# Performance work log

Hardware: AMD Instinct MI355X
Metric: run time of the kernel (lower is better)

Reference implementation:

```python
import jax, jax.numpy as jnp
import numpy as np

DIM = 512
HEADS = 8
DIM_HEAD = 64          # dim // 8
M = 256                # num_landmarks = dim // 2
PINV_ITERS = 6
SCALE = DIM_HEAD ** -0.5
KERNEL = 33            # residual_conv_kernel


def setup_inputs() -> dict:
    key = jax.random.key(0)
    ks = jax.random.split(key, 5)
    b, n = 4, 4096  # n divisible by M -> no padding branch
    inner = HEADS * DIM_HEAD
    x = jax.random.normal(ks[0], (b, n, DIM), jnp.float32)
    ln_w = jnp.ones((DIM,), jnp.float32)
    ln_b = jnp.zeros((DIM,), jnp.float32)
    w_qkv = jax.random.normal(ks[1], (DIM, 3 * inner), jnp.float32) / np.sqrt(DIM)
    w_out = jax.random.normal(ks[2], (inner, DIM), jnp.float32) / np.sqrt(inner)
    b_out = jnp.zeros((DIM,), jnp.float32)
    # depthwise Conv2d(heads, heads, (33,1), groups=heads, bias=False): weight [H,1,33,1]
    w_res = jax.random.normal(ks[3], (HEADS, 1, KERNEL, 1), jnp.float32) * 0.05
    return dict(x=x, ln_w=ln_w, ln_b=ln_b, w_qkv=w_qkv, w_out=w_out, b_out=b_out, w_res=w_res)


def moore_penrose_iter_pinv(x, iters=PINV_ITERS):
    # x: (..., m, m) row-stochastic softmax matrix
    abs_x = jnp.abs(x)
    col = abs_x.sum(-1).max()   # global max, matches torch.max(col)
    row = abs_x.sum(-2).max()
    z = jnp.swapaxes(x, -1, -2) / (col * row)
    I = jnp.eye(x.shape[-1], dtype=x.dtype)
    for _ in range(iters):
        xz = x @ z
        z = 0.25 * z @ (13 * I - xz @ (15 * I - xz @ (7 * I - xz)))
    return z


def reference(x, ln_w, ln_b, w_qkv, w_out, b_out, w_res):
    b, n, d = x.shape
    # pre-norm LayerNorm (eps=1e-5, biased variance)
    mu = x.mean(-1, keepdims=True)
    var = ((x - mu) ** 2).mean(-1, keepdims=True)
    h = (x - mu) * jax.lax.rsqrt(var + 1e-5) * ln_w + ln_b

    qkv = h @ w_qkv                           # (b, n, 3*inner)
    q, k, v = jnp.split(qkv, 3, axis=-1)
    to_heads = lambda t: t.reshape(b, n, HEADS, DIM_HEAD).transpose(0, 2, 1, 3)
    q = to_heads(q) * SCALE                   # (b, h, n, d)
    k = to_heads(k)
    v = to_heads(v)

    # landmarks: mean over consecutive chunks of size l = n // M
    l = n // M
    q_l = q.reshape(b, HEADS, M, l, DIM_HEAD).mean(3)  # (b, h, m, d)
    k_l = k.reshape(b, HEADS, M, l, DIM_HEAD).mean(3)

    sim1 = jnp.einsum('bhid,bhjd->bhij', q, k_l)       # (b, h, n, m)
    sim2 = jnp.einsum('bhid,bhjd->bhij', q_l, k_l)     # (b, h, m, m)
    sim3 = jnp.einsum('bhid,bhjd->bhij', q_l, k)       # (b, h, m, n)
    attn1 = jax.nn.softmax(sim1, -1)
    attn2 = jax.nn.softmax(sim2, -1)
    attn3 = jax.nn.softmax(sim3, -1)

    attn2_inv = moore_penrose_iter_pinv(attn2)
    out = (attn1 @ attn2_inv) @ (attn3 @ v)            # (b, h, n, d)

    # residual depthwise conv over sequence dim, per head
    pad = KERNEL // 2
    res = jax.lax.conv_general_dilated(
        v, w_res, window_strides=(1, 1), padding=((pad, pad), (0, 0)),
        dimension_numbers=('NCHW', 'OIHW', 'NCHW'), feature_group_count=HEADS)
    out = out + res

    out = out.transpose(0, 2, 1, 3).reshape(b, n, HEADS * DIM_HEAD)
    out = out @ w_out + b_out                          # to_out (dropout=identity in eval)
    return x + out
```

## Files before the change

kernel.cpp:

```cpp
#include <hip/hip_runtime.h>
#include <hip/hip_bf16.h>
#include <hip/hip_fp16.h>

#define B_ 4
#define H_ 8
#define N_ 4096
#define DH_ 64
#define D_ 512
#define M_ 256
#define BH_ 32
#define NT_ 16384

typedef unsigned short u16;
using sh8 = __attribute__((ext_vector_type(8))) short;
using sh4 = __attribute__((ext_vector_type(4))) short;
using f4  = __attribute__((ext_vector_type(4))) float;

__device__ __forceinline__ float bf2f(u16 u){ return __uint_as_float(((unsigned)u)<<16); }
__device__ __forceinline__ u16 f2bf(float f){
  unsigned u = __float_as_uint(f);
  u += 0x7fffu + ((u>>16)&1u);
  return (u16)(u>>16);
}

// ... 78 lines not shown
  for (int pass=0; pass<2; pass++){
    __syncthreads();
    if (wr==pass){
      #pragma unroll
      for (int fr=0;fr<4;fr++){
        #pragma unroll
        for (int fc=0;fc<4;fc++){
          #pragma unroll
          for (int j=0;j<4;j++)
            tb[(fr*16+((lane>>4)<<2)+j)*132 + wc*64+fc*16+(lane&15)] = acc[fr][fc][j];
        }
      }
    }
    __syncthreads();
    #pragma unroll
    for (int i=0;i<4;i++){
      int ch = i*256+tid;
      int lr = ch>>4, cq = (ch&15)*8;
      int r = r0 + pass*64 + lr;
      int c = c0 + cq;
      int which = c>>9, hh = (c>>6)&7, d = c&63;
      int bb = r>>12, n = r&4095;
      float scale = (which==0)? 0.125f : 1.f;
      sh8 ov;
      #pragma unroll
      for (int jj=0;jj<8;jj++) ov[jj] = (short)f2bf(tb[lr*132+cq+jj]*scale);
      u16* dst = which==0 ? q : (which==1 ? k : v);
      *(sh8*)(dst + (((size_t)(bb*8+hh))*4096 + n)*64 + d) = ov;
    }
  }
}

__global__ __launch_bounds__(64) void landmark_kernel(const u16* __restrict__ q,
    const u16* __restrict__ k, u16* __restrict__ ql, u16* __restrict__ kl){
  int bh = blockIdx.x, m = blockIdx.y, d = threadIdx.x;
  const u16* qp = q + (((size_t)bh*4096) + m*16)*64 + d;
  const u16* kp = k + (((size_t)bh*4096) + m*16)*64 + d;
  float sq=0, sk=0;
  #pragma unroll
  for (int j=0;j<16;j++){ sq += bf2f(qp[j*64]); sk += bf2f(kp[j*64]); }
  ql[((size_t)bh*256+m)*64+d] = f2bf(sq*(1.f/16.f));
  kl[((size_t)bh*256+m)*64+d] = f2bf(sk*(1.f/16.f));
}

__global__ __launch_bounds__(256) void attn2_kernel(const u16* __restrict__ ql,
    const u16* __restrict__ kl, u16* __restrict__ Xhi, u16* __restrict__ Xlo){
  int bh = blockIdx.x, rb = blockIdx.y;
  __shared__ short klds[256*72];
  const u16* kg = kl + (size_t)bh*256*64;
  int tid = threadIdx.x;
  #pragma unroll
  for (int i=0;i<8;i++){
    int c = i*256+tid, row = c>>3, kgi = c&7;
    *(sh8*)&klds[row*72+kgi*8] = *(const sh8*)(kg + row*64 + kgi*8);
  }
  __syncthreads();
  int r = rb*16 + (tid>>4), t = tid&15;
  const u16* qr = ql + ((size_t)bh*256 + r)*64;
  float qv[64];
  #pragma unroll
  for (int i=0;i<8;i++){
    sh8 v8 = *(const sh8*)(qr + i*8);
    #pragma unroll
    for (int j=0;j<8;j++) qv[i*8+j] = bf2f((u16)v8[j]);
  }
  float s[16];
  #pragma unroll
  for (int j=0;j<16;j++){
    int col = t + 16*j;
    const short* kr = &klds[col*72];
    float accv=0;
    #pragma unroll
    for (int i8=0;i8<8;i8++){
      sh8 kv = *(const sh8*)(kr + i8*8);
      #pragma unroll
      for (int jj=0;jj<8;jj++) accv += qv[i8*8+jj]*bf2f((u16)kv[jj]);
    }
    s[j]=accv;
  }
  float mx = s[0];
  #pragma unroll
  for (int j=1;j<16;j++) mx = fmaxf(mx, s[j]);
  #pragma unroll
  for (int o=1;o<16;o<<=1) mx = fmaxf(mx, __shfl_xor(mx,o));
  float sum=0;
  #pragma unroll
  for (int j=0;j<16;j++){ s[j] = __expf(s[j]-mx); sum += s[j]; }
  #pragma unroll
  for (int o=1;o<16;o<<=1) sum += __shfl_xor(sum,o);
  float inv = 1.f/sum;
  u16* Xh = Xhi + ((size_t)bh*256 + r)*256;
  u16* Xl = Xlo + ((size_t)bh*256 + r)*256;
  #pragma unroll
  for (int j=0;j<16;j++){
    float val = s[j]*inv;
    u16 hb = f2bf(val);
    Xh[t+16*j] = hb; Xl[t+16*j] = f2bf(val - bf2f(hb));
  }
}

__global__ __launch_bounds__(256) void colrow_kernel(const u16* __restrict__ Xhi,
    const u16* __restrict__ Xlo, float* __restrict__ scal){
  int bh = blockIdx.x, t = threadIdx.x;
  const u16* xh = Xhi + (size_t)bh*65536;
  const u16* xl = Xlo + (size_t)bh*65536;
  float cs=0, rs=0;
  for (int m=0;m<256;m++) cs += bf2f(xh[m*256+t]) + bf2f(xl[m*256+t]);
  for (int c=0;c<256;c++) rs += bf2f(xh[t*256+c]) + bf2f(xl[t*256+c]);
  #pragma unroll
  for (int o=32;o;o>>=1){ cs = fmaxf(cs, __shfl_xor(cs,o)); rs = fmaxf(rs, __shfl_xor(rs,o)); }
  __shared__ float sb[4], sb2[4];
  if ((t&63)==0){ sb[t>>6]=cs; sb2[t>>6]=rs; }
  __syncthreads();
  if (t==0){
    float mc = fmaxf(fmaxf(sb[0],sb[1]),fmaxf(sb[2],sb[3]));
    float mr = fmaxf(fmaxf(sb2[0],sb2[1]),fmaxf(sb2[2],sb2[3]));
    atomicMax((unsigned*)&scal[1], __float_as_uint(mc));
    atomicMax((unsigned*)&scal[0], __float_as_uint(mr));
  }
}

__global__ __launch_bounds__(256) void ztinit_kernel(const u16* __restrict__ Xhi,
    const u16* __restrict__ Xlo, const float* __restrict__ scal,
    u16* __restrict__ Zhi, u16* __restrict__ Zlo, u16* __restrict__ ZThi, u16* __restrict__ ZTlo){
  int bh = blockIdx.x; int xr0 = blockIdx.y*64, xc0 = blockIdx.z*64;
  __shared__ float tb[64*66];
  float inv = 1.f/(scal[0]*scal[1]);
  int tid = threadIdx.x;
  size_t mo = (size_t)bh*65536;
  int row = tid>>2, cof = (tid&3)*16;
  #pragma unroll
  for (int s2=0;s2<2;s2++){
    sh8 hv = *(const sh8*)(Xhi + mo + (size_t)(xr0+row)*256 + xc0+cof+s2*8);
    sh8 lv = *(const sh8*)(Xlo + mo + (size_t)(xr0+row)*256 + xc0+cof+s2*8);
    #pragma unroll
    for (int j=0;j<8;j++) tb[row*66 + cof+s2*8+j] = (bf2f((u16)hv[j])+bf2f((u16)lv[j]))*inv;
  }
  __syncthreads();
  int lc = tid&63;
  #pragma unroll
  for (int i=0;i<16;i++){
    int lr = i*4 + (tid>>6);
    float v1 = tb[lr*66+lc];
    u16 h1 = f2bf(v1);
    ZThi[mo + (size_t)(xr0+lr)*256 + xc0+lc] = h1;
    ZTlo[mo + (size_t)(xr0+lr)*256 + xc0+lc] = f2bf(v1 - bf2f(h1));
    float v2 = tb[lc*66+lr];
    u16 h2 = f2bf(v2);
    Zhi[mo + (size_t)(xc0+lr)*256 + xr0+lc] = h2;
    Zlo[mo + (size_t)(xc0+lr)*256 + xr0+lc] = f2bf(v2 - bf2f(h2));
  }
}

__device__ __forceinline__ void pinv_body(
    const u16* __restrict__ Ahi, const u16* __restrict__ Alo,
    const u16* __restrict__ Bthi, const u16* __restrict__ Btlo,
    const u16* __restrict__ E1hi, const u16* __restrict__ E1lo,
    const u16* __restrict__ E2hi, const u16* __restrict__ E2lo,
    u16* __restrict__ Chi, u16* __restrict__ Clo,
    u16* __restrict__ CThi, u16* __restrict__ CTlo,
    float k0, float k1, float k2, int bh, int r0, int col0,
    short* smem){
  size_t mo = (size_t)bh*65536;
  int tid=threadIdx.x, lane=tid&63, w=tid>>6, wr=w>>1, wc=w&1;
  int srow = tid>>2, skof = (tid&3)*8;
  const u16* pA  = Ahi  + mo + (size_t)(r0+srow)*256 + skof;
  const u16* pAl = Alo  + mo + (size_t)(r0+srow)*256 + skof;
  const u16* pB  = Bthi + mo + (size_t)(col0+srow)*256 + skof;
  const u16* pBl = Btlo + mo + (size_t)(col0+srow)*256 + skof;
  float e1v[2][2][4], e2v[2][2][4];
  if (E1hi){
    #pragma unroll
    for (int fr=0;fr<2;fr++){
      #pragma unroll
      for (int fc=0;fc<2;fc++){
        #pragma unroll
        for (int j=0;j<4;j++){
          int lr = wr*32+fr*16+((lane>>4)<<2)+j, lc = wc*32+fc*16+(lane&15);
          size_t o = mo+(size_t)(r0+lr)*256+col0+lc;
          e1v[fr][fc][j] = bf2f(E1hi[o]) + bf2f(E1lo[o]);
        }
      }
    }
  }
  if (E2hi){
    #pragma unroll
    for (int fr=0;fr<2;fr++){
      #pragma unroll
      for (int fc=0;fc<2;fc++){
        #pragma unroll
        for (int j=0;j<4;j++){
          int lr = wr*32+fr*16+((lane>>4)<<2)+j, lc = wc*32+fc*16+(lane&15);
          size_t o = mo+(size_t)(r0+lr)*256+col0+lc;
          e2v[fr][fc][j] = bf2f(E2hi[o]) + bf2f(E2lo[o]);
        }
      }
    }
  }
  sh8 ra  = *(const sh8*)(pA);
  sh8 ral = *(const sh8*)(pAl);
  sh8 rb  = *(const sh8*)(pB);
  sh8 rbl = *(const sh8*)(pBl);
  f4 acc[2][2];
  #pragma unroll
  for (int i=0;i<2;i++){
    #pragma unroll
    for (int j=0;j<2;j++) acc[i][j]=0;
  }
  for (int kt=0;kt<8;kt++){
    short* Ah = smem + (kt&1)*10240;
    short* Al = Ah + 2560; short* Bh = Ah + 5120; short* Bl = Ah + 7680;
    *(sh8*)&Ah[srow*40+skof] = ra;
    *(sh8*)&Al[srow*40+skof] = ral;
    *(sh8*)&Bh[srow*40+skof] = rb;
    *(sh8*)&Bl[srow*40+skof] = rbl;
    __syncthreads();
    if (kt<7){
      int o2 = (kt+1)*32;
      ra  = *(const sh8*)(pA+o2);  ral = *(const sh8*)(pAl+o2);
      rb  = *(const sh8*)(pB+o2);  rbl = *(const sh8*)(pBl+o2);
    }
    sh8 ah[2], al[2], bh8[2], bl8[2];
    #pragma unroll
    for (int fr=0;fr<2;fr++){
      int off = (wr*32+fr*16+(lane&15))*40 + ((lane>>4)<<3);
      ah[fr] = *(const sh8*)&Ah[off]; al[fr] = *(const sh8*)&Al[off];
    }
    #pragma unroll
    for (int fc=0;fc<2;fc++){
      int off = (wc*32+fc*16+(lane&15))*40 + ((lane>>4)<<3);
      bh8[fc] = *(const sh8*)&Bh[off]; bl8[fc] = *(const sh8*)&Bl[off];
    }
    #pragma unroll
    for (int fr=0;fr<2;fr++){
      #pragma unroll
      for (int fc=0;fc<2;fc++){
        acc[fr][fc] = __builtin_amdgcn_mfma_f32_16x16x32_bf16(ah[fr], bh8[fc], acc[fr][fc], 0,0,0);
        acc[fr][fc] = __builtin_amdgcn_mfma_f32_16x16x32_bf16(ah[fr], bl8[fc], acc[fr][fc], 0,0,0);
        acc[fr][fc] = __builtin_amdgcn_mfma_f32_16x16x32_bf16(al[fr], bh8[fc], acc[fr][fc], 0,0,0);
      }
    }
  }
  __syncthreads();
  float* tb = (float*)smem;
  #pragma unroll
  for (int fr=0;fr<2;fr++){
    #pragma unroll
    for (int fc=0;fc<2;fc++){
      #pragma unroll
      for (int j=0;j<4;j++){
        int lr = wr*32+fr*16+((lane>>4)<<2)+j, lc = wc*32+fc*16+(lane&15);
        float val = k0*acc[fr][fc][j];
        if (E1hi) val += k1*e1v[fr][fc][j];
        if (E2hi) val += k2*e2v[fr][fc][j];
        tb[lr*66+lc] = val;
      }
    }
  }
  __syncthreads();
  int lc2 = tid&63;
  #pragma unroll
  for (int i=0;i<16;i++){
    int lr2 = i*4+(tid>>6);
    if (Chi){
      float v1 = tb[lr2*66+lc2];
      u16 hb=f2bf(v1);
      Chi[mo+(size_t)(r0+lr2)*256+col0+lc2]=hb;
      Clo[mo+(size_t)(r0+lr2)*256+col0+lc2]=f2bf(v1-bf2f(hb));
    }
    if (CThi){
      float v2 = tb[lc2*66 + lr2];
      u16 hb2=f2bf(v2);
      CThi[mo+(size_t)(col0+lr2)*256 + r0+lc2]=hb2;
      CTlo[mo+(size_t)(col0+lr2)*256 + r0+lc2]=f2bf(v2-bf2f(hb2));
    }
  }
}

__global__ __launch_bounds__(256) void pinv_mm(
    const u16* Ahi, const u16* Alo, const u16* Bthi, const u16* Btlo,
    const u16* E1hi, const u16* E1lo, const u16* E2hi, const u16* E2lo,
    u16* Chi, u16* Clo, u16* CThi, u16* CTlo,
    float k0, float k1, float k2){
  __shared__ __align__(16) short smem[2*10240];
  pinv_body(Ahi,Alo,Bthi,Btlo,E1hi,E1lo,E2hi,E2lo,Chi,Clo,CThi,CTlo,
            k0,k1,k2, blockIdx.z, blockIdx.x*64, blockIdx.y*64, smem);
}

__global__ __launch_bounds__(256) void pinv_zupd(
    const u16* Zhi, const u16* Zlo, u16* ZnHi, u16* ZnLo,
    const u16* T1hi, const u16* T1lo,
    u16* TnChi, u16* TnClo, u16* TnThi, u16* TnTlo,
    const u16* Bthi, const u16* Btlo){
  __shared__ __align__(16) short smem[2*10240];
  int which = blockIdx.z >> 5, bh = blockIdx.z & 31;
  const u16* Ah = which ? T1hi : Zhi;
  const u16* Al = which ? T1lo : Zlo;
  u16* Ch  = which ? TnChi : ZnHi;
  u16* Cl  = which ? TnClo : ZnLo;
  u16* CTh = which ? TnThi : (u16*)0;
  u16* CTl = which ? TnTlo : (u16*)0;
  pinv_body(Ah,Al,Bthi,Btlo, Ah,Al, (u16*)0,(u16*)0, Ch,Cl,CTh,CTl,
            -0.25f, 3.25f, 0.f, bh, blockIdx.x*64, blockIdx.y*64, smem);
}

__global__ __launch_bounds__(256) void gemm_logits(const u16* __restrict__ Aall,
    const u16* __restrict__ Btall, __half* __restrict__ Oall,
    int N, size_t sA, size_t sB, size_t sO){
  int bh = blockIdx.z;
  const u16* A  = Aall  + (size_t)bh*sA + (size_t)blockIdx.x*128*64;
  const u16* Bt = Btall + (size_t)bh*sB + (size_t)blockIdx.y*128*64;
  __half* O = Oall + (size_t)bh*sO + (size_t)blockIdx.x*128*N + (size_t)blockIdx.y*128;
  __shared__ short As[128*72], Bs[128*72];
  int tid=threadIdx.x, lane=tid&63, w=tid>>6, wr=w>>1, wc=w&1;
  #pragma unroll
  for (int i=0;i<4;i++){
    int c=i*256+tid, row=c>>3, kg=c&7;
    *(sh8*)&As[row*72+kg*8] = *(const sh8*)(A  + (size_t)row*64 + kg*8);
    *(sh8*)&Bs[row*72+kg*8] = *(const sh8*)(Bt + (size_t)row*64 + kg*8);
  }
  __syncthreads();
  f4 acc[4][4];
  #pragma unroll
  for (int i=0;i<4;i++){
    #pragma unroll
    for (int j=0;j<4;j++) acc[i][j]=0;
  }
  #pragma unroll
  for (int kc=0;kc<2;kc++){
    sh8 a[4], bq[4];
    #pragma unroll
    for (int fr=0;fr<4;fr++) a[fr]  = *(const sh8*)&As[(wr*64+fr*16+(lane&15))*72 + kc*32 + ((lane>>4)<<3)];
    #pragma unroll
    for (int fc=0;fc<4;fc++) bq[fc] = *(const sh8*)&Bs[(wc*64+fc*16+(lane&15))*72 + kc*32 + ((lane>>4)<<3)];
    #pragma unroll
    for (int fr=0;fr<4;fr++){
      #pragma unroll
      for (int fc=0;fc<4;fc++)
        acc[fr][fc] = __builtin_amdgcn_mfma_f32_16x16x32_bf16(a[fr], bq[fc], acc[fr][fc], 0,0,0);
    }
  }
  #pragma unroll
  for (int fr=0;fr<4;fr++){
    #pragma unroll
    for (int fc=0;fc<4;fc++){
      #pragma unroll
      for (int j=0;j<4;j++)
        O[(size_t)(wr*64+fr*16+((lane>>4)<<2)+j)*N + wc*64+fc*16+(lane&15)] = __float2half(acc[fr][fc][j]);
    }
  }
}

__global__ __launch_bounds__(256) void stats_kernel(const __half* __restrict__ logits,
    float2* __restrict__ stats, int RL){
  size_t row = blockIdx.x;
  const __half2* p = (const __half2*)(logits + row*RL);
  int t = threadIdx.x, n2 = RL>>1;
  float mx = -1e30f;
  for (int i=t;i<n2;i+=256){ float2 f = __half22float2(p[i]); mx = fmaxf(mx, fmaxf(f.x,f.y)); }
  #pragma unroll
  for (int o=32;o;o>>=1) mx = fmaxf(mx, __shfl_xor(mx,o));
  __shared__ float sb[4], sb2[4];
  if ((t&63)==0) sb[t>>6]=mx;
  __syncthreads();
  mx = fmaxf(fmaxf(sb[0],sb[1]),fmaxf(sb[2],sb[3]));
  float s=0;
  for (int i=t;i<n2;i+=256){ float2 f = __half22float2(p[i]); s += __expf(f.x-mx)+__expf(f.y-mx); }
  #pragma unroll
  for (int o=32;o;o>>=1) s += __shfl_xor(s,o);
  if ((t&63)==0) sb2[t>>6]=s;
  __syncthreads();
  s = sb2[0]+sb2[1]+sb2[2]+sb2[3];
  if (t==0) stats[row] = make_float2(mx, 1.f/s);
}

__global__ __launch_bounds__(256) void gemm_out3(const __half* __restrict__ Lall,
    const float2* __restrict__ stall, const u16* __restrict__ vall, float* __restrict__ part){
  int bh = blockIdx.z, mt = blockIdx.x, ks = blockIdx.y;
  const __half* L = Lall + (size_t)bh*256*4096 + (size_t)mt*128*4096 + (size_t)ks*512;
  const float2* st = stall + (size_t)bh*256 + mt*128;
  const u16* V = vall + (size_t)bh*4096*64 + (size_t)ks*512*64;
  float* O = part + ((size_t)(bh*8+ks)*256 + (size_t)mt*128)*64;
  __shared__ short As[128*72], Bs[64*72];
  int tid=threadIdx.x, lane=tid&63, w=tid>>6;
  f4 acc[2][4];
  #pragma unroll
  for (int i=0;i<2;i++){
    #pragma unroll
    for (int j=0;j<4;j++) acc[i][j]=0;
  }
  for (int kt=0;kt<8;kt++){
    __syncthreads();
    #pragma unroll
    for (int i=0;i<4;i++){
      int c=i*256+tid, row=c>>3, kg=c&7;
      const __half2* src = (const __half2*)(L + (size_t)row*4096 + kt*64 + kg*8);
      float2 ms = st[row];
      sh8 ov;
      #pragma unroll
      for (int jj=0;jj<4;jj++){
        float2 f = __half22float2(src[jj]);
        ov[2*jj]   = (short)f2bf(__expf(f.x-ms.x)*ms.y);
        ov[2*jj+1] = (short)f2bf(__expf(f.y-ms.x)*ms.y);
      }
      *(sh8*)&As[row*72+kg*8] = ov;
    }
    #pragma unroll
    for (int i=0;i<16;i++){
      int c=i*256+tid, d=c&63, nl=c>>6;
      Bs[d*72+nl] = (short)V[(size_t)(kt*64+nl)*64 + d];
    }
    __syncthreads();
    #pragma unroll
    for (int kc=0;kc<2;kc++){
      sh8 a[2], bq[4];
      #pragma unroll
      for (int fr=0;fr<2;fr++) a[fr]  = *(const sh8*)&As[(w*32+fr*16+(lane&15))*72 + kc*32+((lane>>4)<<3)];
      #pragma unroll
      for (int fc=0;fc<4;fc++) bq[fc] = *(const sh8*)&Bs[(fc*16+(lane&15))*72 + kc*32+((lane>>4)<<3)];
      #pragma unroll
      for (int fr=0;fr<2;fr++){
        #pragma unroll
        for (int fc=0;fc<4;fc++)
          acc[fr][fc] = __builtin_amdgcn_mfma_f32_16x16x32_bf16(a[fr], bq[fc], acc[fr][fc], 0,0,0);
      }
    }
  }
  #pragma unroll
  for (int fr=0;fr<2;fr++){
    #pragma unroll
    for (int fc=0;fc<4;fc++){
      #pragma unroll
      for (int j=0;j<4;j++)
        O[(size_t)(w*32+fr*16+((lane>>4)<<2)+j)*64 + fc*16+(lane&15)] = acc[fr][fc][j];
    }
  }
}

__global__ __launch_bounds__(256) void reduce_o3(const float* __restrict__ part, float* __restrict__ o3){
  int idx = blockIdx.x*256+threadIdx.x;
  int bh = idx>>14, rem = idx & 16383;
  float s=0;
  #pragma unroll
  for (int ks=0;ks<8;ks++) s += part[(((size_t)(bh*8+ks))<<14) + rem];
  o3[idx]=s;
}

__global__ __launch_bounds__(256) void wt_kernel(const u16* __restrict__ Zhi,
    const u16* __restrict__ Zlo, const float* __restrict__ o3, u16* __restrict__ Wt){
  int bh = blockIdx.x; int m = blockIdx.y*4 + (threadIdx.x>>6); int d = threadIdx.x&63;
  const u16* zh = Zhi + ((size_t)bh*256 + m)*256;
  const u16* zl = Zlo + ((size_t)bh*256 + m)*256;
  const float* op = o3 + (size_t)bh*256*64 + d;
  float accv = 0;
  for (int kk=0;kk<256;kk++) accv += (bf2f(zh[kk])+bf2f(zl[kk]))*op[kk*64];
  Wt[((size_t)bh*64 + d)*256 + m] = f2bf(accv);
}

__global__ __launch_bounds__(256) void fused_out1(const u16* __restrict__ q,
    const u16* __restrict__ klall, const u16* __restrict__ Wtall, u16* __restrict__ Oall){
  int rb = blockIdx.x, bh = blockIdx.y;
  __shared__ __align__(16) short sm[18432];
  short* Bs = sm; short* P = sm;
  int tid=threadIdx.x, lane=tid&63, w=tid>>6;
  const u16* qb  = q + ((size_t)bh*4096 + (size_t)rb*64)*64;
  const u16* klb = klall + (size_t)bh*256*64;
  const u16* Wt  = Wtall + (size_t)bh*64*256;
  #pragma unroll
  for (int i=0;i<8;i++){
    int c = i*256+tid, row = c>>3, kg = c&7;
    *(sh8*)&Bs[row*72+kg*8] = *(const sh8*)(klb + row*64 + kg*8);
  }
  const u16* qrow = qb + (size_t)(w*16+(lane&15))*64 + ((lane>>4)<<3);
  sh8 a0 = *(const sh8*)(qrow);
  sh8 a1 = *(const sh8*)(qrow + 32);
  __syncthreads();
  f4 acc[16];
  #pragma unroll
  for (int fc=0;fc<16;fc++){
    sh8 b0 = *(const sh8*)&Bs[(fc*16+(lane&15))*72 + ((lane>>4)<<3)];
    sh8 b1 = *(const sh8*)&Bs[(fc*16+(lane&15))*72 + 32 + ((lane>>4)<<3)];
    acc[fc]=0;
    acc[fc] = __builtin_amdgcn_mfma_f32_16x16x32_bf16(a0, b0, acc[fc], 0,0,0);
    acc[fc] = __builtin_amdgcn_mfma_f32_16x16x32_bf16(a1, b1, acc[fc], 0,0,0);
  }
  float inv_[4];
  #pragma unroll
  for (int j=0;j<4;j++){
    float mx=-1e30f;
    #pragma unroll
    for (int fc=0;fc<16;fc++) mx = fmaxf(mx, acc[fc][j]);
    #pragma unroll
    for (int o=1;o<16;o<<=1) mx = fmaxf(mx, __shfl_xor(mx,o));
    float s=0;
    #pragma unroll
    for (int fc=0;fc<16;fc++){ float e=__expf(acc[fc][j]-mx); acc[fc][j]=e; s+=e; }
    #pragma unroll
    for (int o=1;o<16;o<<=1) s += __shfl_xor(s,o);
    inv_[j] = 1.f/s;
  }
  __syncthreads();
  #pragma unroll
  for (int fc=0;fc<16;fc++){
    #pragma unroll
    for (int j=0;j<4;j++){
      int row = w*16 + ((lane>>4)<<2) + j, col = fc*16 + (lane&15);
      P[row*268 + col] = (short)f2bf(acc[fc][j]*inv_[j]);
    }
  }
  __syncthreads();
  f4 acc2[4];
  #pragma unroll
  for (int fc2=0;fc2<4;fc2++) acc2[fc2]=0;
  sh8 bqA[4], bqB[4];
  #pragma unroll
  for (int fc2=0;fc2<4;fc2++){
    int d = fc2*16 + (lane&15);
    bqA[fc2] = *(const sh8*)(Wt + (size_t)d*256 + ((lane>>4))*8);
  }
  #pragma unroll
  for (int kp=0;kp<4;kp++){
    int kc0 = kp*2, kc1 = kp*2+1;
    #pragma unroll
    for (int fc2=0;fc2<4;fc2++){
      int d = fc2*16 + (lane&15);
      bqB[fc2] = *(const sh8*)(Wt + (size_t)d*256 + (kc1*4+(lane>>4))*8);
    }
    sh8 a = *(const sh8*)&P[(w*16+(lane&15))*268 + kc0*32 + ((lane>>4)<<3)];
    #pragma unroll
    for (int fc2=0;fc2<4;fc2++)
      acc2[fc2] = __builtin_amdgcn_mfma_f32_16x16x32_bf16(a, bqA[fc2], acc2[fc2], 0,0,0);
    if (kp<3){
      #pragma unroll
      for (int fc2=0;fc2<4;fc2++){
        int d = fc2*16 + (lane&15);
        bqA[fc2] = *(const sh8*)(Wt + (size_t)d*256 + ((kc1+1)*4+(lane>>4))*8);
      }
    }
    sh8 a2 = *(const sh8*)&P[(w*16+(lane&15))*268 + kc1*32 + ((lane>>4)<<3)];
    #pragma unroll
    for (int fc2=0;fc2<4;fc2++)
      acc2[fc2] = __builtin_amdgcn_mfma_f32_16x16x32_bf16(a2, bqB[fc2], acc2[fc2], 0,0,0);
  }
  __syncthreads();
  u16* otb = (u16*)sm;
  #pragma unroll
  for (int fc2=0;fc2<4;fc2++){
    #pragma unroll
    for (int j=0;j<4;j++)
      otb[(w*16+((lane>>4)<<2)+j)*72 + fc2*16+(lane&15)] = f2bf(acc2[fc2][j]);
  }
  __syncthreads();
  u16* O = Oall + ((size_t)bh*4096 + (size_t)rb*64)*64;
  #pragma unroll
  for (int i=0;i<2;i++){
    int ch = i*256+tid; int lr = ch>>3, cq = (ch&7)*8;
    sh8 ov = *(sh8*)&otb[lr*72+cq];
    *(sh8*)(O + (size_t)lr*64 + cq) = ov;
  }
}

__global__ __launch_bounds__(256) void combine_kernel(const u16* __restrict__ out1,
    const u16* __restrict__ v, const float* __restrict__ wres, u16* __restrict__ oc){
  int bh = blockIdx.x; int hh = bh&7, bb = bh>>3;
  int n0 = blockIdx.y*64;
  int tid = threadIdx.x, d = tid&63, sub = tid>>6;
  int nbase = n0 + sub*16;
  const u16* vb = v + ((size_t)bh*4096)*64 + d;
  float w_[33];
  #pragma unroll
  for (int j=0;j<33;j++) w_[j] = wres[hh*33+j];
  float vv[48];
  #pragma unroll
  for (int i=0;i<48;i++){
    int nn = nbase + i - 16;
    vv[i] = (nn>=0 && nn<4096) ? bf2f(vb[(size_t)nn*64]) : 0.f;
  }
  #pragma unroll
  for (int r=0;r<16;r++){
    int n = nbase + r;
    float acc = bf2f(out1[(((size_t)bh*4096)+n)*64 + d]);
    #pragma unroll
    for (int j=0;j<33;j++) acc += w_[j]*vv[r+j];
    oc[((size_t)(bb*4096+n))*512 + hh*64 + d] = f2bf(acc);
  }
}

__global__ __launch_bounds__(256) void gemm_final(const u16* __restrict__ A,
    const u16* __restrict__ Bt, const float* __restrict__ x, const float* __restrict__ bo,
    float* __restrict__ out){
  __shared__ short As[128*72], Bs[128*72];
  int r0 = blockIdx.x*128, c0 = blockIdx.y*128;
  int tid = threadIdx.x, lane = tid&63, w = tid>>6;
  int wr = w>>1, wc = w&1;
  f4 acc[4][4];
  #pragma unroll
  for (int i=0;i<4;i++){
    #pragma unroll
    for (int j=0;j<4;j++) acc[i][j]=0;
  }
  for (int kt=0;kt<8;kt++){
    __syncthreads();
    #pragma unroll
    for (int i=0;i<4;i++){
      int c = i*256+tid, row = c>>3, kg = c&7;
      *(sh8*)&As[row*72+kg*8] = *(const sh8*)(A  + (size_t)(r0+row)*512 + kt*64 + kg*8);
      *(sh8*)&Bs[row*72+kg*8] = *(const sh8*)(Bt + (size_t)(c0+row)*512 + kt*64 + kg*8);
    }
    __syncthreads();
    #pragma unroll
    for (int kc=0;kc<2;kc++){
      sh8 a[4], bq[4];
      #pragma unroll
      for (int fr=0;fr<4;fr++) a[fr]  = *(const sh8*)&As[(wr*64+fr*16+(lane&15))*72 + kc*32 + ((lane>>4)<<3)];
      #pragma unroll
      for (int fc=0;fc<4;fc++) bq[fc] = *(const sh8*)&Bs[(wc*64+fc*16+(lane&15))*72 + kc*32 + ((lane>>4)<<3)];
      #pragma unroll
      for (int fr=0;fr<4;fr++){
        #pragma unroll
        for (int fc=0;fc<4;fc++)
          acc[fr][fc] = __builtin_amdgcn_mfma_f32_16x16x32_bf16(a[fr], bq[fc], acc[fr][fc], 0,0,0);
      }
    }
  }
  #pragma unroll
  for (int fr=0;fr<4;fr++){
    #pragma unroll
    for (int fc=0;fc<4;fc++){
      #pragma unroll
      for (int j=0;j<4;j++){
        int r = r0 + wr*64 + fr*16 + ((lane>>4)<<2) + j;
        int c = c0 + wc*64 + fc*16 + (lane&15);
        out[(size_t)r*512+c] = x[(size_t)r*512+c] + acc[fr][fc][j] + bo[c];
      }
    }
  }
}

extern "C" void kernel_launch(void* const* d_in, const int* in_sizes, int n_in,
                              void* d_out, int out_size, void* d_ws, size_t ws_size,
                              hipStream_t stream){
  const float* x    = (const float*)d_in[0];
  const float* lnw  = (const float*)d_in[1];
  const float* lnb  = (const float*)d_in[2];
  const float* wqkv = (const float*)d_in[3];
  const float* wout = (const float*)d_in[4];
  const float* bout = (const float*)d_in[5];
  const float* wres = (const float*)d_in[6];
  float* out = (float*)d_out;

  char* ws = (char*)d_ws;
  size_t off = 0;
  auto alloc = [&](size_t bytes)->void*{ void* p = ws + off; off += (bytes + 255) & ~(size_t)255; return p; };
  u16* h      = (u16*)alloc((size_t)NT_*512*2);
  u16* wqkvT  = (u16*)alloc((size_t)1536*512*2);
  u16* woutT  = (u16*)alloc((size_t)512*512*2);
  u16* k      = (u16*)alloc((size_t)BH_*4096*64*2);
  u16* v      = (u16*)alloc((size_t)BH_*4096*64*2);
  u16* q      = (u16*)alloc((size_t)BH_*4096*64*2);
  float* part = (float*)alloc((size_t)BH_*8*256*64*4);
  u16* ql     = (u16*)alloc((size_t)BH_*256*64*2);
  u16* kl     = (u16*)alloc((size_t)BH_*256*64*2);
  u16* ZaChi  = (u16*)alloc((size_t)BH_*65536*2);
  u16* ZaClo  = (u16*)alloc((size_t)BH_*65536*2);
  u16* ZbChi  = (u16*)alloc((size_t)BH_*65536*2);
  u16* ZbClo  = (u16*)alloc((size_t)BH_*65536*2);
  __half* logits = (__half*)alloc((size_t)BH_*4096*256*2);
  float2* st3 = (float2*)alloc((size_t)BH_*256*8);
  float* o3   = (float*)alloc((size_t)BH_*256*64*4);
  u16* Wt     = (u16*)alloc((size_t)BH_*64*256*2);
  float* scal = (float*)alloc(256);
  u16* out1   = (u16*)logits;
  u16* oc     = h;

  const size_t C1 = (size_t)BH_*65536;
  u16* base = (u16*)logits;
  u16* Xhi   = base + 0*C1;  u16* Xlo   = base + 1*C1;
  u16* T1aCh = base + 2*C1;  u16* T1aCl = base + 3*C1;
  u16* T1aTh = base + 4*C1;  u16* T1aTl = base + 5*C1;
  u16* T1bCh = base + 6*C1;  u16* T1bCl = base + 7*C1;
  u16* T1bTh = base + 8*C1;  u16* T1bTl = base + 9*C1;
  u16* SCh   = base +10*C1;  u16* SCl   = base +11*C1;
  u16* STh   = base +12*C1;  u16* STl   = base +13*C1;
  u16* T3h   = base +14*C1;  u16* T3l   = base +15*C1;
  u16* Z0Th  = SCh;          u16* Z0Tl  = SCl;

  ln_kernel<<<NT_, 256, 0, stream>>>(x, lnw, lnb, h);
  castT2_kernel<<<(512*1536+512*512+255)/256, 256, 0, stream>>>(wqkv, wqkvT, wout, woutT);
  gemm_qkv<<<dim3(128,12,1), 256, 0, stream>>>(h, wqkvT, q, k, v);
  landmark_kernel<<<dim3(32,256,1), 64, 0, stream>>>(q, k, ql, kl);
  attn2_kernel<<<dim3(32,16,1), 256, 0, stream>>>(ql, kl, Xhi, Xlo);
  hipMemsetAsync(scal, 0, 8, stream);
  colrow_kernel<<<32, 256, 0, stream>>>(Xhi, Xlo, scal);
  ztinit_kernel<<<dim3(32,4,4), 256, 0, stream>>>(Xhi, Xlo, scal, ZaChi, ZaClo, Z0Th, Z0Tl);

  u16* nul = (u16*)0;
  pinv_mm<<<dim3(4,4,32),256,0,stream>>>(Xhi,Xlo, Z0Th,Z0Tl, nul,nul,nul,nul,
      T1aCh,T1aCl, T1aTh,T1aTl, 1.f,0.f,0.f);
  u16 *TcCh=T1aCh,*TcCl=T1aCl,*TcTh=T1aTh,*TcTl=T1aTl;
  u16 *TnCh=T1bCh,*TnCl=T1bCl,*TnTh=T1bTh,*TnTl=T1bTl;
  u16 *Zch=ZaChi,*Zcl=ZaClo, *Znh=ZbChi,*Znl=ZbClo;
  for (int it=0; it<6; it++){
    pinv_mm<<<dim3(4,4,32),256,0,stream>>>(TcCh,TcCl, TcTh,TcTl, nul,nul,nul,nul,
        SCh,SCl, STh,STl, 1.f,0.f,0.f);
    pinv_mm<<<dim3(4,4,32),256,0,stream>>>(TcCh,TcCl, STh,STl, TcCh,TcCl, SCh,SCl,
        nul,nul, T3h,T3l, 1.f,15.f,-7.f);
    if (it<5){
      pinv_zupd<<<dim3(4,4,64),256,0,stream>>>(Zch,Zcl, Znh,Znl,
          TcCh,TcCl, TnCh,TnCl, TnTh,TnTl, T3h,T3l);
      u16* t;
      t=Zch;Zch=Znh;Znh=t; t=Zcl;Zcl=Znl;Znl=t;
      t=TcCh;TcCh=TnCh;TnCh=t; t=TcCl;TcCl=TnCl;TnCl=t;
      t=TcTh;TcTh=TnTh;TnTh=t; t=TcTl;TcTl=TnTl;TnTl=t;
    } else {
      pinv_mm<<<dim3(4,4,32),256,0,stream>>>(Zch,Zcl, T3h,T3l, Zch,Zcl, nul,nul,
          Znh,Znl, nul,nul, -0.25f,3.25f,0.f);
    }
  }

  gemm_logits<<<dim3(2,32,32),256,0,stream>>>(ql, k, logits, 4096,
      (size_t)256*64, (size_t)4096*64, (size_t)256*4096);
  stats_kernel<<<BH_*256, 256, 0, stream>>>(logits, st3, 4096);
  gemm_out3<<<dim3(2,8,32),256,0,stream>>>(logits, st3, v, part);
  reduce_o3<<<2048, 256, 0, stream>>>(part, o3);
  wt_kernel<<<dim3(32,64,1),256,0,stream>>>(ZaChi, ZaClo, o3, Wt);
  fused_out1<<<dim3(64,32,1),256,0,stream>>>(q, kl, Wt, out1);
  combine_kernel<<<dim3(32,64,1),256,0,stream>>>(out1, v, wres, oc);
  gemm_final<<<dim3(128,4,1),256,0,stream>>>(oc, woutT, x, bout, out);
}
```

Baseline: 611.4 us.

## Fuse attn3 path into flash-style kernel and use low-precision early pinv iterations

```diff
diff --git a/kernel.cpp b/kernel.cpp
--- a/kernel.cpp
+++ b/kernel.cpp
@@ -254,6 +254,7 @@
   }
 }
 
+template<int LO>
 __device__ __forceinline__ void pinv_body(
     const u16* __restrict__ Ahi, const u16* __restrict__ Alo,
     const u16* __restrict__ Bthi, const u16* __restrict__ Btlo,
@@ -280,7 +281,7 @@
         for (int j=0;j<4;j++){
           int lr = wr*32+fr*16+((lane>>4)<<2)+j, lc = wc*32+fc*16+(lane&15);
           size_t o = mo+(size_t)(r0+lr)*256+col0+lc;
-          e1v[fr][fc][j] = bf2f(E1hi[o]) + bf2f(E1lo[o]);
+          e1v[fr][fc][j] = bf2f(E1hi[o]) + (LO ? bf2f(E1lo[o]) : 0.f);
         }
       }
     }
@@ -294,15 +295,15 @@
         for (int j=0;j<4;j++){
           int lr = wr*32+fr*16+((lane>>4)<<2)+j, lc = wc*32+fc*16+(lane&15);
           size_t o = mo+(size_t)(r0+lr)*256+col0+lc;
-          e2v[fr][fc][j] = bf2f(E2hi[o]) + bf2f(E2lo[o]);
+          e2v[fr][fc][j] = bf2f(E2hi[o]) + (LO ? bf2f(E2lo[o]) : 0.f);
         }
       }
     }
   }
   sh8 ra  = *(const sh8*)(pA);
-  sh8 ral = *(const sh8*)(pAl);
   sh8 rb  = *(const sh8*)(pB);
-  sh8 rbl = *(const sh8*)(pBl);
+  sh8 ral{}, rbl{};
+  if (LO){ ral = *(const sh8*)(pAl); rbl = *(const sh8*)(pBl); }
   f4 acc[2][2];
   #pragma unroll
   for (int i=0;i<2;i++){
@@ -313,33 +314,39 @@
     short* Ah = smem + (kt&1)*10240;
     short* Al = Ah + 2560; short* Bh = Ah + 5120; short* Bl = Ah + 7680;
     *(sh8*)&Ah[srow*40+skof] = ra;
-    *(sh8*)&Al[srow*40+skof] = ral;
     *(sh8*)&Bh[srow*40+skof] = rb;
-    *(sh8*)&Bl[srow*40+skof] = rbl;
+    if (LO){
+      *(sh8*)&Al[srow*40+skof] = ral;
+      *(sh8*)&Bl[srow*40+skof] = rbl;
+    }
     __syncthreads();
     if (kt<7){
       int o2 = (kt+1)*32;
-      ra  = *(const sh8*)(pA+o2);  ral = *(const sh8*)(pAl+o2);
-      rb  = *(const sh8*)(pB+o2);  rbl = *(const sh8*)(pBl+o2);
+      ra  = *(const sh8*)(pA+o2);  rb  = *(const sh8*)(pB+o2);
+      if (LO){ ral = *(const sh8*)(pAl+o2); rbl = *(const sh8*)(pBl+o2); }
     }
     sh8 ah[2], al[2], bh8[2], bl8[2];
     #pragma unroll
     for (int fr=0;fr<2;fr++){
       int off = (wr*32+fr*16+(lane&15))*40 + ((lane>>4)<<3);
-      ah[fr] = *(const sh8*)&Ah[off]; al[fr] = *(const sh8*)&Al[off];
+      ah[fr] = *(const sh8*)&Ah[off];
+      if (LO) al[fr] = *(const sh8*)&Al[off];
     }
     #pragma unroll
     for (int fc=0;fc<2;fc++){
       int off = (wc*32+fc*16+(lane&15))*40 + ((lane>>4)<<3);
-      bh8[fc] = *(const sh8*)&Bh[off]; bl8[fc] = *(const sh8*)&Bl[off];
+      bh8[fc] = *(const sh8*)&Bh[off];
+      if (LO) bl8[fc] = *(const sh8*)&Bl[off];
     }
     #pragma unroll
     for (int fr=0;fr<2;fr++){
       #pragma unroll
       for (int fc=0;fc<2;fc++){
         acc[fr][fc] = __builtin_amdgcn_mfma_f32_16x16x32_bf16(ah[fr], bh8[fc], acc[fr][fc], 0,0,0);
-        acc[fr][fc] = __builtin_amdgcn_mfma_f32_16x16x32_bf16(ah[fr], bl8[fc], acc[fr][fc], 0,0,0);
-        acc[fr][fc] = __builtin_amdgcn_mfma_f32_16x16x32_bf16(al[fr], bh8[fc], acc[fr][fc], 0,0,0);
+        if (LO){
+          acc[fr][fc] = __builtin_amdgcn_mfma_f32_16x16x32_bf16(ah[fr], bl8[fc], acc[fr][fc], 0,0,0);
+          acc[fr][fc] = __builtin_amdgcn_mfma_f32_16x16x32_bf16(al[fr], bh8[fc], acc[fr][fc], 0,0,0);
+        }
       }
     }
   }
@@ -379,152 +386,143 @@
   }
 }
 
+template<int LO>
 __global__ __launch_bounds__(256) void pinv_mm(
     const u16* Ahi, const u16* Alo, const u16* Bthi, const u16* Btlo,
     const u16* E1hi, const u16* E1lo, const u16* E2hi, const u16* E2lo,
     u16* Chi, u16* Clo, u16* CThi, u16* CTlo,
     float k0, float k1, float k2){
   __shared__ __align__(16) short smem[2*10240];
-  pinv_body(Ahi,Alo,Bthi,Btlo,E1hi,E1lo,E2hi,E2lo,Chi,Clo,CThi,CTlo,
+  pinv_body<LO>(Ahi,Alo,Bthi,Btlo,E1hi,E1lo,E2hi,E2lo,Chi,Clo,CThi,CTlo,
             k0,k1,k2, blockIdx.z, blockIdx.x*64, blockIdx.y*64, smem);
 }
 
+template<int LO>
 __global__ __launch_bounds__(256) void pinv_zupd(
     const u16* Zhi, const u16* Zlo, u16* ZnHi, u16* ZnLo,
     const u16* T1hi, const u16* T1lo,
     u16* TnChi, u16* TnClo, u16* TnThi, u16* TnTlo,
-    const u16* Bthi, const u16* Btlo){
+    const u16* Bthi, const u16* Btlo,
+    u16* ZTh, u16* ZTl){
   __shared__ __align__(16) short smem[2*10240];
   int which = blockIdx.z >> 5, bh = blockIdx.z & 31;
   const u16* Ah = which ? T1hi : Zhi;
   const u16* Al = which ? T1lo : Zlo;
   u16* Ch  = which ? TnChi : ZnHi;
   u16* Cl  = which ? TnClo : ZnLo;
-  u16* CTh = which ? TnThi : (u16*)0;
-  u16* CTl = which ? TnTlo : (u16*)0;
-  pinv_body(Ah,Al,Bthi,Btlo, Ah,Al, (u16*)0,(u16*)0, Ch,Cl,CTh,CTl,
+  u16* CTh = which ? TnThi : ZTh;
+  u16* CTl = which ? TnTlo : ZTl;
+  pinv_body<LO>(Ah,Al,Bthi,Btlo, Ah,Al, (u16*)0,(u16*)0, Ch,Cl,CTh,CTl,
             -0.25f, 3.25f, 0.f, bh, blockIdx.x*64, blockIdx.y*64, smem);
 }
 
-__global__ __launch_bounds__(256) void gemm_logits(const u16* __restrict__ Aall,
-    const u16* __restrict__ Btall, __half* __restrict__ Oall,
-    int N, size_t sA, size_t sB, size_t sO){
-  int bh = blockIdx.z;
-  const u16* A  = Aall  + (size_t)bh*sA + (size_t)blockIdx.x*128*64;
-  const u16* Bt = Btall + (size_t)bh*sB + (size_t)blockIdx.y*128*64;
-  __half* O = Oall + (size_t)bh*sO + (size_t)blockIdx.x*128*N + (size_t)blockIdx.y*128;
-  __shared__ short As[128*72], Bs[128*72];
-  int tid=threadIdx.x, lane=tid&63, w=tid>>6, wr=w>>1, wc=w&1;
-  #pragma unroll
-  for (int i=0;i<4;i++){
-    int c=i*256+tid, row=c>>3, kg=c&7;
-    *(sh8*)&As[row*72+kg*8] = *(const sh8*)(A  + (size_t)row*64 + kg*8);
-    *(sh8*)&Bs[row*72+kg*8] = *(const sh8*)(Bt + (size_t)row*64 + kg*8);
-  }
-  __syncthreads();
-  f4 acc[4][4];
-  #pragma unroll
-  for (int i=0;i<4;i++){
-    #pragma unroll
-    for (int j=0;j<4;j++) acc[i][j]=0;
-  }
-  #pragma unroll
-  for (int kc=0;kc<2;kc++){
-    sh8 a[4], bq[4];
-    #pragma unroll
-    for (int fr=0;fr<4;fr++) a[fr]  = *(const sh8*)&As[(wr*64+fr*16+(lane&15))*72 + kc*32 + ((lane>>4)<<3)];
-    #pragma unroll
-    for (int fc=0;fc<4;fc++) bq[fc] = *(const sh8*)&Bs[(wc*64+fc*16+(lane&15))*72 + kc*32 + ((lane>>4)<<3)];
-    #pragma unroll
-    for (int fr=0;fr<4;fr++){
-      #pragma unroll
-      for (int fc=0;fc<4;fc++)
-        acc[fr][fc] = __builtin_amdgcn_mfma_f32_16x16x32_bf16(a[fr], bq[fc], acc[fr][fc], 0,0,0);
-    }
-  }
-  #pragma unroll
-  for (int fr=0;fr<4;fr++){
-    #pragma unroll
-    for (int fc=0;fc<4;fc++){
-      #pragma unroll
-      for (int j=0;j<4;j++)
-        O[(size_t)(wr*64+fr*16+((lane>>4)<<2)+j)*N + wc*64+fc*16+(lane&15)] = __float2half(acc[fr][fc][j]);
-    }
-  }
-}
-
-__global__ __launch_bounds__(256) void stats_kernel(const __half* __restrict__ logits,
-    float2* __restrict__ stats, int RL){
-  size_t row = blockIdx.x;
-  const __half2* p = (const __half2*)(logits + row*RL);
-  int t = threadIdx.x, n2 = RL>>1;
-  float mx = -1e30f;
-  for (int i=t;i<n2;i+=256){ float2 f = __half22float2(p[i]); mx = fmaxf(mx, fmaxf(f.x,f.y)); }
-  #pragma unroll
-  for (int o=32;o;o>>=1) mx = fmaxf(mx, __shfl_xor(mx,o));
-  __shared__ float sb[4], sb2[4];
-  if ((t&63)==0) sb[t>>6]=mx;
-  __syncthreads();
-  mx = fmaxf(fmaxf(sb[0],sb[1]),fmaxf(sb[2],sb[3]));
-  float s=0;
-  for (int i=t;i<n2;i+=256){ float2 f = __half22float2(p[i]); s += __expf(f.x-mx)+__expf(f.y-mx); }
-  #pragma unroll
-  for (int o=32;o;o>>=1) s += __shfl_xor(s,o);
-  if ((t&63)==0) sb2[t>>6]=s;
-  __syncthreads();
-  s = sb2[0]+sb2[1]+sb2[2]+sb2[3];
-  if (t==0) stats[row] = make_float2(mx, 1.f/s);
-}
-
-__global__ __launch_bounds__(256) void gemm_out3(const __half* __restrict__ Lall,
-    const float2* __restrict__ stall, const u16* __restrict__ vall, float* __restrict__ part){
-  int bh = blockIdx.z, mt = blockIdx.x, ks = blockIdx.y;
-  const __half* L = Lall + (size_t)bh*256*4096 + (size_t)mt*128*4096 + (size_t)ks*512;
-  const float2* st = stall + (size_t)bh*256 + mt*128;
-  const u16* V = vall + (size_t)bh*4096*64 + (size_t)ks*512*64;
+__global__ __launch_bounds__(256) void flash_out3(const u16* __restrict__ qlall,
+    const u16* __restrict__ kall, const u16* __restrict__ vall,
+    float* __restrict__ part, float2* __restrict__ pms){
+  int mt = blockIdx.x, ks = blockIdx.y, bh = blockIdx.z;
+  const u16* QL = qlall + ((size_t)bh*256 + mt*128)*64;
+  const u16* K  = kall + ((size_t)bh*4096 + (size_t)ks*512)*64;
+  const u16* V  = vall + ((size_t)bh*4096 + (size_t)ks*512)*64;
   float* O = part + ((size_t)(bh*8+ks)*256 + (size_t)mt*128)*64;
-  __shared__ short As[128*72], Bs[64*72];
+  float2* MS = pms + (size_t)(bh*8+ks)*256 + mt*128;
+  __shared__ __align__(16) short kls[64*72];
+  __shared__ __align__(16) short vts[64*72];
+  __shared__ __align__(16) short Pls[128*72];
   int tid=threadIdx.x, lane=tid&63, w=tid>>6;
-  f4 acc[2][4];
-  #pragma unroll
-  for (int i=0;i<2;i++){
-    #pragma unroll
-    for (int j=0;j<4;j++) acc[i][j]=0;
+  sh8 aq[2][2];
+  #pragma unroll
+  for (int fr=0;fr<2;fr++){
+    #pragma unroll
+    for (int kc=0;kc<2;kc++)
+      aq[fr][kc] = *(const sh8*)(QL + (size_t)(w*32+fr*16+(lane&15))*64 + kc*32 + ((lane>>4)<<3));
+  }
+  f4 oacc[2][4];
+  #pragma unroll
+  for (int fr=0;fr<2;fr++){
+    #pragma unroll
+    for (int fc=0;fc<4;fc++) oacc[fr][fc]=0;
+  }
+  float mrun[2][4], srun[2][4];
+  #pragma unroll
+  for (int fr=0;fr<2;fr++){
+    #pragma unroll
+    for (int j=0;j<4;j++){ mrun[fr][j]=-1e30f; srun[fr][j]=0.f; }
   }
   for (int kt=0;kt<8;kt++){
     __syncthreads();
     #pragma unroll
-    for (int i=0;i<4;i++){
+    for (int i=0;i<2;i++){
       int c=i*256+tid, row=c>>3, kg=c&7;
-      const __half2* src = (const __half2*)(L + (size_t)row*4096 + kt*64 + kg*8);
-      float2 ms = st[row];
-      sh8 ov;
-      #pragma unroll
-      for (int jj=0;jj<4;jj++){
-        float2 f = __half22float2(src[jj]);
-        ov[2*jj]   = (short)f2bf(__expf(f.x-ms.x)*ms.y);
-        ov[2*jj+1] = (short)f2bf(__expf(f.y-ms.x)*ms.y);
-      }
-      *(sh8*)&As[row*72+kg*8] = ov;
+      *(sh8*)&kls[row*72+kg*8] = *(const sh8*)(K + (size_t)(kt*64+row)*64 + kg*8);
     }
     #pragma unroll
     for (int i=0;i<16;i++){
       int c=i*256+tid, d=c&63, nl=c>>6;
-      Bs[d*72+nl] = (short)V[(size_t)(kt*64+nl)*64 + d];
+      vts[d*72+nl] = (short)V[(size_t)(kt*64+nl)*64 + d];
     }
     __syncthreads();
+    f4 sacc[2][4];
+    #pragma unroll
+    for (int fr=0;fr<2;fr++){
+      #pragma unroll
+      for (int fc=0;fc<4;fc++) sacc[fr][fc]=0;
+    }
     #pragma unroll
     for (int kc=0;kc<2;kc++){
-      sh8 a[2], bq[4];
-      #pragma unroll
-      for (int fr=0;fr<2;fr++) a[fr]  = *(const sh8*)&As[(w*32+fr*16+(lane&15))*72 + kc*32+((lane>>4)<<3)];
-      #pragma unroll
-      for (int fc=0;fc<4;fc++) bq[fc] = *(const sh8*)&Bs[(fc*16+(lane&15))*72 + kc*32+((lane>>4)<<3)];
+      sh8 bk[4];
+      #pragma unroll
+      for (int fc=0;fc<4;fc++) bk[fc] = *(const sh8*)&kls[(fc*16+(lane&15))*72 + kc*32 + ((lane>>4)<<3)];
       #pragma unroll
       for (int fr=0;fr<2;fr++){
         #pragma unroll
         for (int fc=0;fc<4;fc++)
-          acc[fr][fc] = __builtin_amdgcn_mfma_f32_16x16x32_bf16(a[fr], bq[fc], acc[fr][fc], 0,0,0);
+          sacc[fr][fc] = __builtin_amdgcn_mfma_f32_16x16x32_bf16(aq[fr][kc], bk[fc], sacc[fr][fc], 0,0,0);
+      }
+    }
+    #pragma unroll
+    for (int fr=0;fr<2;fr++){
+      #pragma unroll
+      for (int j=0;j<4;j++){
+        float mt_ = fmaxf(fmaxf(sacc[fr][0][j],sacc[fr][1][j]), fmaxf(sacc[fr][2][j],sacc[fr][3][j]));
+        #pragma unroll
+        for (int o=1;o<16;o<<=1) mt_ = fmaxf(mt_, __shfl_xor(mt_,o));
+        float mnew = fmaxf(mrun[fr][j], mt_);
+        float scale = __expf(mrun[fr][j]-mnew);
+        float e0 = __expf(sacc[fr][0][j]-mnew);
+        float e1 = __expf(sacc[fr][1][j]-mnew);
+        float e2 = __expf(sacc[fr][2][j]-mnew);
+        float e3 = __expf(sacc[fr][3][j]-mnew);
+        sacc[fr][0][j]=e0; sacc[fr][1][j]=e1; sacc[fr][2][j]=e2; sacc[fr][3][j]=e3;
+        float sum = (e0+e1)+(e2+e3);
+        #pragma unroll
+        for (int o=1;o<16;o<<=1) sum += __shfl_xor(sum,o);
+        srun[fr][j] = srun[fr][j]*scale + sum;
+        mrun[fr][j] = mnew;
+        #pragma unroll
+        for (int fc=0;fc<4;fc++) oacc[fr][fc][j] *= scale;
+      }
+    }
+    #pragma unroll
+    for (int fr=0;fr<2;fr++){
+      #pragma unroll
+      for (int fc=0;fc<4;fc++){
+        #pragma unroll
+        for (int j=0;j<4;j++)
+          Pls[(w*32+fr*16+((lane>>4)<<2)+j)*72 + fc*16+(lane&15)] = (short)f2bf(sacc[fr][fc][j]);
+      }
+    }
+    #pragma unroll
+    for (int kc=0;kc<2;kc++){
+      sh8 pa[2], bv[4];
+      #pragma unroll
+      for (int fr=0;fr<2;fr++) pa[fr] = *(const sh8*)&Pls[(w*32+fr*16+(lane&15))*72 + kc*32 + ((lane>>4)<<3)];
+      #pragma unroll
+      for (int fc=0;fc<4;fc++) bv[fc] = *(const sh8*)&vts[(fc*16+(lane&15))*72 + kc*32 + ((lane>>4)<<3)];
+      #pragma unroll
+      for (int fr=0;fr<2;fr++){
+        #pragma unroll
+        for (int fc=0;fc<4;fc++)
+          oacc[fr][fc] = __builtin_amdgcn_mfma_f32_16x16x32_bf16(pa[fr], bv[fc], oacc[fr][fc], 0,0,0);
       }
     }
   }
@@ -534,18 +532,38 @@
     for (int fc=0;fc<4;fc++){
       #pragma unroll
       for (int j=0;j<4;j++)
-        O[(size_t)(w*32+fr*16+((lane>>4)<<2)+j)*64 + fc*16+(lane&15)] = acc[fr][fc][j];
-    }
-  }
-}
-
-__global__ __launch_bounds__(256) void reduce_o3(const float* __restrict__ part, float* __restrict__ o3){
+        O[(size_t)(w*32+fr*16+((lane>>4)<<2)+j)*64 + fc*16+(lane&15)] = oacc[fr][fc][j];
+    }
+  }
+  if ((lane&15)==0){
+    #pragma unroll
+    for (int fr=0;fr<2;fr++){
+      #pragma unroll
+      for (int j=0;j<4;j++)
+        MS[w*32+fr*16+((lane>>4)<<2)+j] = make_float2(mrun[fr][j], srun[fr][j]);
+    }
+  }
+}
+
+__global__ __launch_bounds__(256) void reduce_o3(const float* __restrict__ part,
+    const float2* __restrict__ pms, float* __restrict__ o3){
   int idx = blockIdx.x*256+threadIdx.x;
-  int bh = idx>>14, rem = idx & 16383;
-  float s=0;
-  #pragma unroll
-  for (int ks=0;ks<8;ks++) s += part[(((size_t)(bh*8+ks))<<14) + rem];
-  o3[idx]=s;
+  int d = idx&63, row = (idx>>6)&255, bh = idx>>14;
+  float2 ms[8];
+  float M = -1e30f;
+  #pragma unroll
+  for (int ks=0;ks<8;ks++){
+    ms[ks] = pms[(size_t)(bh*8+ks)*256 + row];
+    M = fmaxf(M, ms[ks].x);
+  }
+  float S=0.f, acc=0.f;
+  #pragma unroll
+  for (int ks=0;ks<8;ks++){
+    float e = __expf(ms[ks].x - M);
+    S += e*ms[ks].y;
+    acc += e*part[((size_t)(bh*8+ks)*256 + row)*64 + d];
+  }
+  o3[idx] = acc/S;
 }
 
 __global__ __launch_bounds__(256) void wt_kernel(const u16* __restrict__ Zhi,
@@ -589,14 +607,18 @@
   float inv_[4];
   #pragma unroll
   for (int j=0;j<4;j++){
-    float mx=-1e30f;
-    #pragma unroll
-    for (int fc=0;fc<16;fc++) mx = fmaxf(mx, acc[fc][j]);
+    float m0 = fmaxf(fmaxf(acc[0][j],acc[1][j]), fmaxf(acc[2][j],acc[3][j]));
+    float m1 = fmaxf(fmaxf(acc[4][j],acc[5][j]), fmaxf(acc[6][j],acc[7][j]));
+    float m2 = fmaxf(fmaxf(acc[8][j],acc[9][j]), fmaxf(acc[10][j],acc[11][j]));
+    float m3 = fmaxf(fmaxf(acc[12][j],acc[13][j]), fmaxf(acc[14][j],acc[15][j]));
+    float mx = fmaxf(fmaxf(m0,m1), fmaxf(m2,m3));
     #pragma unroll
     for (int o=1;o<16;o<<=1) mx = fmaxf(mx, __shfl_xor(mx,o));
-    float s=0;
-    #pragma unroll
-    for (int fc=0;fc<16;fc++){ float e=__expf(acc[fc][j]-mx); acc[fc][j]=e; s+=e; }
+    float e[16];
+    #pragma unroll
+    for (int fc=0;fc<16;fc++){ e[fc]=__expf(acc[fc][j]-mx); acc[fc][j]=e[fc]; }
+    float s = (((e[0]+e[1])+(e[2]+e[3])) + ((e[4]+e[5])+(e[6]+e[7])))
+            + (((e[8]+e[9])+(e[10]+e[11])) + ((e[12]+e[13])+(e[14]+e[15])));
     #pragma unroll
     for (int o=1;o<16;o<<=1) s += __shfl_xor(s,o);
     inv_[j] = 1.f/s;
@@ -761,22 +783,22 @@
   u16* v      = (u16*)alloc((size_t)BH_*4096*64*2);
   u16* q      = (u16*)alloc((size_t)BH_*4096*64*2);
   float* part = (float*)alloc((size_t)BH_*8*256*64*4);
+  float2* pms = (float2*)alloc((size_t)BH_*8*256*8);
   u16* ql     = (u16*)alloc((size_t)BH_*256*64*2);
   u16* kl     = (u16*)alloc((size_t)BH_*256*64*2);
   u16* ZaChi  = (u16*)alloc((size_t)BH_*65536*2);
   u16* ZaClo  = (u16*)alloc((size_t)BH_*65536*2);
   u16* ZbChi  = (u16*)alloc((size_t)BH_*65536*2);
   u16* ZbClo  = (u16*)alloc((size_t)BH_*65536*2);
-  __half* logits = (__half*)alloc((size_t)BH_*4096*256*2);
-  float2* st3 = (float2*)alloc((size_t)BH_*256*8);
+  u16* scratch = (u16*)alloc((size_t)BH_*65536*2*16);
   float* o3   = (float*)alloc((size_t)BH_*256*64*4);
   u16* Wt     = (u16*)alloc((size_t)BH_*64*256*2);
   float* scal = (float*)alloc(256);
-  u16* out1   = (u16*)logits;
+  u16* out1   = scratch;
   u16* oc     = h;
 
   const size_t C1 = (size_t)BH_*65536;
-  u16* base = (u16*)logits;
+  u16* base = scratch;
   u16* Xhi   = base + 0*C1;  u16* Xlo   = base + 1*C1;
   u16* T1aCh = base + 2*C1;  u16* T1aCl = base + 3*C1;
   u16* T1aTh = base + 4*C1;  u16* T1aTl = base + 5*C1;
@@ -786,6 +808,7 @@
   u16* STh   = base +12*C1;  u16* STl   = base +13*C1;
   u16* T3h   = base +14*C1;  u16* T3l   = base +15*C1;
   u16* Z0Th  = SCh;          u16* Z0Tl  = SCl;
+  u16* ZTth  = (u16*)part;   u16* ZTtl  = ZTth + C1;
 
   ln_kernel<<<NT_, 256, 0, stream>>>(x, lnw, lnb, h);
   castT2_kernel<<<(512*1536+512*512+255)/256, 256, 0, stream>>>(wqkv, wqkvT, wout, woutT);
@@ -797,34 +820,50 @@
   ztinit_kernel<<<dim3(32,4,4), 256, 0, stream>>>(Xhi, Xlo, scal, ZaChi, ZaClo, Z0Th, Z0Tl);
 
   u16* nul = (u16*)0;
-  pinv_mm<<<dim3(4,4,32),256,0,stream>>>(Xhi,Xlo, Z0Th,Z0Tl, nul,nul,nul,nul,
+  pinv_mm<1><<<dim3(4,4,32),256,0,stream>>>(Xhi,Xlo, Z0Th,Z0Tl, nul,nul,nul,nul,
       T1aCh,T1aCl, T1aTh,T1aTl, 1.f,0.f,0.f);
   u16 *TcCh=T1aCh,*TcCl=T1aCl,*TcTh=T1aTh,*TcTl=T1aTl;
   u16 *TnCh=T1bCh,*TnCl=T1bCl,*TnTh=T1bTh,*TnTl=T1bTl;
   u16 *Zch=ZaChi,*Zcl=ZaClo, *Znh=ZbChi,*Znl=ZbClo;
   for (int it=0; it<6; it++){
-    pinv_mm<<<dim3(4,4,32),256,0,stream>>>(TcCh,TcCl, TcTh,TcTl, nul,nul,nul,nul,
-        SCh,SCl, STh,STl, 1.f,0.f,0.f);
-    pinv_mm<<<dim3(4,4,32),256,0,stream>>>(TcCh,TcCl, STh,STl, TcCh,TcCl, SCh,SCl,
-        nul,nul, T3h,T3l, 1.f,15.f,-7.f);
+    if (it==4){
+      pinv_mm<1><<<dim3(4,4,32),256,0,stream>>>(Xhi,Xlo, ZTth,ZTtl, nul,nul,nul,nul,
+          TnCh,TnCl, TnTh,TnTl, 1.f,0.f,0.f);
+      u16* t;
+      t=TcCh;TcCh=TnCh;TnCh=t; t=TcCl;TcCl=TnCl;TnCl=t;
+      t=TcTh;TcTh=TnTh;TnTh=t; t=TcTl;TcTl=TnTl;TnTl=t;
+    }
+    if (it<4){
+      pinv_mm<0><<<dim3(4,4,32),256,0,stream>>>(TcCh,TcCl, TcTh,TcTl, nul,nul,nul,nul,
+          SCh,SCl, STh,STl, 1.f,0.f,0.f);
+      pinv_mm<0><<<dim3(4,4,32),256,0,stream>>>(TcCh,TcCl, STh,STl, TcCh,TcCl, SCh,SCl,
+          nul,nul, T3h,T3l, 1.f,15.f,-7.f);
+    } else {
+      pinv_mm<1><<<dim3(4,4,32),256,0,stream>>>(TcCh,TcCl, TcTh,TcTl, nul,nul,nul,nul,
+          SCh,SCl, STh,STl, 1.f,0.f,0.f);
+      pinv_mm<1><<<dim3(4,4,32),256,0,stream>>>(TcCh,TcCl, STh,STl, TcCh,TcCl, SCh,SCl,
+          nul,nul, T3h,T3l, 1.f,15.f,-7.f);
+    }
     if (it<5){
-      pinv_zupd<<<dim3(4,4,64),256,0,stream>>>(Zch,Zcl, Znh,Znl,
-          TcCh,TcCl, TnCh,TnCl, TnTh,TnTl, T3h,T3l);
+      if (it<4)
+        pinv_zupd<0><<<dim3(4,4,64),256,0,stream>>>(Zch,Zcl, Znh,Znl,
+            TcCh,TcCl, TnCh,TnCl, TnTh,TnTl, T3h,T3l,
+            (it==3)?ZTth:nul, (it==3)?ZTtl:nul);
+      else
+        pinv_zupd<1><<<dim3(4,4,64),256,0,stream>>>(Zch,Zcl, Znh,Znl,
+            TcCh,TcCl, TnCh,TnCl, TnTh,TnTl, T3h,T3l, nul, nul);
       u16* t;
       t=Zch;Zch=Znh;Znh=t; t=Zcl;Zcl=Znl;Znl=t;
       t=TcCh;TcCh=TnCh;TnCh=t; t=TcCl;TcCl=TnCl;TnCl=t;
       t=TcTh;TcTh=TnTh;TnTh=t; t=TcTl;TcTl=TnTl;TnTl=t;
     } else {
-      pinv_mm<<<dim3(4,4,32),256,0,stream>>>(Zch,Zcl, T3h,T3l, Zch,Zcl, nul,nul,
+      pinv_mm<1><<<dim3(4,4,32),256,0,stream>>>(Zch,Zcl, T3h,T3l, Zch,Zcl, nul,nul,
           Znh,Znl, nul,nul, -0.25f,3.25f,0.f);
     }
   }
 
-  gemm_logits<<<dim3(2,32,32),256,0,stream>>>(ql, k, logits, 4096,
-      (size_t)256*64, (size_t)4096*64, (size_t)256*4096);
-  stats_kernel<<<BH_*256, 256, 0, stream>>>(logits, st3, 4096);
-  gemm_out3<<<dim3(2,8,32),256,0,stream>>>(logits, st3, v, part);
-  reduce_o3<<<2048, 256, 0, stream>>>(part, o3);
+  flash_out3<<<dim3(2,8,32),256,0,stream>>>(ql, k, v, part, pms);
+  reduce_o3<<<2048, 256, 0, stream>>>(part, pms, o3);
   wt_kernel<<<dim3(32,64,1),256,0,stream>>>(ZaChi, ZaClo, o3, Wt);
   fused_out1<<<dim3(64,32,1),256,0,stream>>>(q, kl, Wt, out1);
   combine_kernel<<<dim3(32,64,1),256,0,stream>>>(out1, v, wres, oc);
```

New measurement: 536.1 us. 12.3% less time.
